# Optimization experiments

Measured on AMD Instinct MI355X. Metric: run time of the kernel, lower is better.

## Reference

```python
import jax, jax.numpy as jnp
import numpy as np

N1 = 4097
N2 = 8192


def setup_inputs() -> dict:
    key = jax.random.key(0)
    kx, ka, kb, km = jax.random.split(key, 4)
    x = jax.random.normal(kx, ((N1 - 1) * N2 + 1,), dtype=jnp.float32)
    a = jax.random.uniform(ka, (1,), dtype=jnp.float32)
    b = jax.random.uniform(kb, (N2, N1 - 1), dtype=jnp.float32)
    mu = jax.random.uniform(km, (1,), dtype=jnp.float32)
    return {"x": x, "a": a, "b": b, "mu": mu}


def reference(x, a, b, mu):
    n2, n1m1 = b.shape  # (n2, n1-1)
    n1 = n1m1 + 1
    # y = x[1 : (n1-1)*n2 + 1].reshape(n2, n1-1)
    y = x[1:(n1 - 1) * n2 + 1].reshape(n2, n1 - 1)
    # Original loop: i in range(n1-2), j in range(n2-1); term uses y[j, i-1],
    # which at i=0 wraps to the LAST column (negative indexing). Reproduce via roll.
    y_cur = y[: n2 - 1, : n1 - 2]                       # y[j, i]
    y_prev = jnp.roll(y, 1, axis=1)[: n2 - 1, : n1 - 2]  # y[j, i-1] with wraparound
    terms = b[: n2 - 1, : n1 - 2] * (y_cur - y_prev ** 2) ** 2
    return -a * (x[0] - mu) ** 2 - jnp.sum(terms)
```

## Files before the change

kernel.cpp:

```cpp
#include <hip/hip_runtime.h>


#define ROWLEN 4096
#define NCOLS  4095
#define NROWS  8191

__global__ __launch_bounds__(256) void rosen_partial(const float* __restrict__ x,
                                                     const float* __restrict__ b,
                                                     float* __restrict__ partial) {
    const int row = blockIdx.x;
    const float* __restrict__ xr = x + 1 + (size_t)row * ROWLEN;
    const float* __restrict__ br = b + (size_t)row * ROWLEN;

    const float wrap = xr[ROWLEN - 1];

    float acc = 0.0f;
    for (int j = threadIdx.x; j < NCOLS; j += 256) {
        float cur  = xr[j];
        float prev = (j == 0) ? wrap : xr[j - 1];
        float d = cur - prev * prev;
        acc += br[j] * d * d;
    }

    #pragma unroll
    for (int off = 32; off > 0; off >>= 1)
        acc += __shfl_down(acc, off, 64);

    __shared__ float s[4];
    const int lane = threadIdx.x & 63;
    const int wid  = threadIdx.x >> 6;
    if (lane == 0) s[wid] = acc;
    __syncthreads();
    if (threadIdx.x == 0)
        partial[row] = s[0] + s[1] + s[2] + s[3];
}

__global__ __launch_bounds__(256) void rosen_final(const float* __restrict__ partial,
                                                   const float* __restrict__ x,
                                                   const float* __restrict__ a,
                                                   const float* __restrict__ mu,
                                                   float* __restrict__ out) {
    float acc = 0.0f;
    for (int i = threadIdx.x; i < NROWS; i += 256)
        acc += partial[i];

    #pragma unroll
    for (int off = 32; off > 0; off >>= 1)
        acc += __shfl_down(acc, off, 64);

    __shared__ float s[4];
    const int lane = threadIdx.x & 63;
    const int wid  = threadIdx.x >> 6;
    if (lane == 0) s[wid] = acc;
    __syncthreads();
    if (threadIdx.x == 0) {
        float total = s[0] + s[1] + s[2] + s[3];
        float d = x[0] - mu[0];
        out[0] = -a[0] * d * d - total;
    }
}

extern "C" void kernel_launch(void* const* d_in, const int* in_sizes, int n_in,
                              void* d_out, int out_size, void* d_ws, size_t ws_size,
                              hipStream_t stream) {
    const float* x  = (const float*)d_in[0];
    const float* a  = (const float*)d_in[1];
    const float* b  = (const float*)d_in[2];
    const float* mu = (const float*)d_in[3];
    float* out = (float*)d_out;
    float* partial = (float*)d_ws;

    rosen_partial<<<NROWS, 256, 0, stream>>>(x, b, partial);
    rosen_final<<<1, 256, 0, stream>>>(partial, x, a, mu, out);
}
```

Before: 285.1 us.

## Flatten into grid-stride float4 streaming with register prefetch of next group

Replaces one-block-per-row scalar loads with a persistent grid of 2048 blocks. Each thread processes 8 contiguous elements per pass using float4 loads for both x and b, and software-prefetches the next group's data into registers before computing the current one. Row boundaries are handled with masks on the group index: a wrap value is loaded at row starts and the last column's weight is zeroed. The aim is to raise memory-level parallelism and cut the number of load instructions, at the cost of more registers and an unaligned scalar load per group.

```diff
diff --git a/kernel.cpp b/kernel.cpp
--- a/kernel.cpp
+++ b/kernel.cpp
@@ -1,25 +1,64 @@
 #include <hip/hip_runtime.h>
 
 
-#define ROWLEN 4096
-#define NCOLS  4095
-#define NROWS  8191
+#define TOTAL   (8191u * 4096u)
+#define GROUPS  (TOTAL / 8u)
+#define GRID    2048
+#define BLOCK   256
+#define NTHREAD (GRID * BLOCK)
+#define NPASS   ((GROUPS + NTHREAD - 1) / NTHREAD)
 
-__global__ __launch_bounds__(256) void rosen_partial(const float* __restrict__ x,
-                                                     const float* __restrict__ b,
-                                                     float* __restrict__ partial) {
-    const int row = blockIdx.x;
-    const float* __restrict__ xr = x + 1 + (size_t)row * ROWLEN;
-    const float* __restrict__ br = b + (size_t)row * ROWLEN;
+__global__ __launch_bounds__(BLOCK) void rosen_partial(const float* __restrict__ x,
+                                                       const float* __restrict__ b,
+                                                       float* __restrict__ partial) {
+    const unsigned tid = blockIdx.x * BLOCK + threadIdx.x;
+    const float4* __restrict__ x4 = (const float4*)x;
+    const float4* __restrict__ b4 = (const float4*)b;
 
-    const float wrap = xr[ROWLEN - 1];
+    unsigned g = tid;
+    bool cvalid = true;
+    size_t e = (size_t)g * 8;
+    float4 cp0 = x4[e >> 2], cp1 = x4[(e >> 2) + 1];
+    float  cs  = x[e + 8];
+    float4 cb0 = b4[e >> 2], cb1 = b4[(e >> 2) + 1];
+    float  cw  = 0.0f;
+    if ((g & 511u) == 0u) cw = x[e + 4096];
 
     float acc = 0.0f;
-    for (int j = threadIdx.x; j < NCOLS; j += 256) {
-        float cur  = xr[j];
-        float prev = (j == 0) ? wrap : xr[j - 1];
-        float d = cur - prev * prev;
-        acc += br[j] * d * d;
+
+    #pragma unroll 1
+    for (int pass = 0; pass < NPASS; ++pass) {
+        unsigned gn = g + NTHREAD;
+        bool nvalid = (gn < GROUPS);
+        unsigned gl = nvalid ? gn : g;
+        size_t en = (size_t)gl * 8;
+        float4 np0 = x4[en >> 2], np1 = x4[(en >> 2) + 1];
+        float  ns  = x[en + 8];
+        float4 nb0 = b4[en >> 2], nb1 = b4[(en >> 2) + 1];
+        float  nw  = 0.0f;
+        if ((gl & 511u) == 0u) nw = x[en + 4096];
+
+        if (cvalid) {
+            float px = cp0.x;
+            if ((g & 511u) == 0u)   px = cw;
+            if ((g & 511u) == 511u) cb1.w = 0.0f;
+
+            float d0 = cp0.y - px    * px;
+            float d1 = cp0.z - cp0.y * cp0.y;
+            float d2 = cp0.w - cp0.z * cp0.z;
+            float d3 = cp1.x - cp0.w * cp0.w;
+            float d4 = cp1.y - cp1.x * cp1.x;
+            float d5 = cp1.z - cp1.y * cp1.y;
+            float d6 = cp1.w - cp1.z * cp1.z;
+            float d7 = cs    - cp1.w * cp1.w;
+            acc += cb0.x * d0 * d0 + cb0.y * d1 * d1
+                 + cb0.z * d2 * d2 + cb0.w * d3 * d3
+                 + cb1.x * d4 * d4 + cb1.y * d5 * d5
+                 + cb1.z * d6 * d6 + cb1.w * d7 * d7;
+        }
+
+        g = gn; cvalid = nvalid;
+        cp0 = np0; cp1 = np1; cs = ns; cb0 = nb0; cb1 = nb1; cw = nw;
     }
 
     #pragma unroll
@@ -32,7 +71,7 @@
     if (lane == 0) s[wid] = acc;
     __syncthreads();
     if (threadIdx.x == 0)
-        partial[row] = s[0] + s[1] + s[2] + s[3];
+        partial[blockIdx.x] = s[0] + s[1] + s[2] + s[3];
 }
 
 __global__ __launch_bounds__(256) void rosen_final(const float* __restrict__ partial,
@@ -41,7 +80,7 @@
                                                    const float* __restrict__ mu,
                                                    float* __restrict__ out) {
     float acc = 0.0f;
-    for (int i = threadIdx.x; i < NROWS; i += 256)
+    for (int i = threadIdx.x; i < GRID; i += 256)
         acc += partial[i];
 
     #pragma unroll
@@ -70,6 +109,6 @@
     float* out = (float*)d_out;
     float* partial = (float*)d_ws;
 
-    rosen_partial<<<NROWS, 256, 0, stream>>>(x, b, partial);
+    rosen_partial<<<GRID, BLOCK, 0, stream>>>(x, b, partial);
     rosen_final<<<1, 256, 0, stream>>>(partial, x, a, mu, out);
 }
```

Result: faster. 278.6 us (-2.3%).
